# Optimization experiments

Measured on AMD Instinct MI355X. Metric: run time of the kernel, lower is better.

Reference implementation:

```python
import jax, jax.numpy as jnp
import numpy as np

K = 32        # num_classes
NQ = 16384    # num query samples
C = 512       # feature_dim
H_REF = 512   # refinement_net hidden
H_CONF = 256  # confidence_net hidden
NUM_STEPS = 3


def setup_inputs() -> dict:
    key = jax.random.key(0)
    ks = jax.random.split(key, 8)
    s = 0.02
    return {
        "prototypes": jax.random.normal(ks[0], (K, C), jnp.float32),
        "query_features": jax.random.normal(ks[1], (NQ, C), jnp.float32),
        "query_distances": jax.random.uniform(ks[2], (NQ, K), jnp.float32) * 10.0,
        "W1": jax.random.normal(ks[3], (2 * C, H_REF), jnp.float32) * s,
        "b1": jnp.zeros((H_REF,), jnp.float32),
        "W2": jax.random.normal(ks[4], (H_REF, C), jnp.float32) * s,
        "b2": jnp.zeros((C,), jnp.float32),
        "Wc1": jax.random.normal(ks[5], (2 * C, H_CONF), jnp.float32) * s,
        "bc1": jnp.zeros((H_CONF,), jnp.float32),
        "Wc2": jax.random.normal(ks[6], (H_CONF, 1), jnp.float32) * s,
        "bc2": jnp.zeros((1,), jnp.float32),
    }


def reference(prototypes, query_features, query_distances,
              W1, b1, W2, b2, Wc1, bc1, Wc2, bc2):
    # ---- refinement loop (3 steps, sequential in refined prototypes) ----
    refined = prototypes
    for step in range(NUM_STEPS):
        # soft assignments over classes; temperature = step + 1
        soft = jax.nn.softmax(-query_distances / (step + 1.0), axis=-1)  # (NQ, K)
        wsum = jnp.maximum(soft.sum(axis=0), 1e-6)                       # (K,)  clamp(min=1e-6)
        wmean = (soft.T @ query_features) / wsum[:, None]                # (K, C)
        concat = jnp.concatenate([refined, wmean], axis=-1)              # (K, 2C)
        h = jax.nn.relu(concat @ W1 + b1)                                # dropout is identity in eval
        refinement = h @ W2 + b2                                         # (K, C)
        refined = refined + 0.1 * refinement

    # ---- confidence scores: MLP on [proto, query] pairs, mean over queries ----
    # Split first-layer weight into proto half and query half to avoid
    # materializing the (K, NQ, 2C) concat explicitly (same math).
    Wp, Wq = Wc1[:C], Wc1[C:]
    hp = prototypes @ Wp          # (K, H_CONF)
    hq = query_features @ Wq      # (NQ, H_CONF)
    hidden = jax.nn.relu(hp[:, None, :] + hq[None, :, :] + bc1)  # (K, NQ, H_CONF)
    conf = jax.nn.sigmoid(hidden @ Wc2 + bc2)                    # (K, NQ, 1)
    confidence_scores = conf.reshape(K, -1).mean(axis=1)         # (K,)

    return refined, confidence_scores
```

## Files before the change

### kernel.cpp

```cpp
#include <hip/hip_runtime.h>

typedef __attribute__((ext_vector_type(8))) short short8;
typedef __attribute__((ext_vector_type(4))) short short4_t;
typedef __attribute__((ext_vector_type(8))) __bf16 bf16x8;
typedef __attribute__((ext_vector_type(4))) float floatx4;

union S8B8 { short8 s; bf16x8 b; };

__device__ __forceinline__ short f2bf(float f) {
    union { float f; unsigned u; } v; v.f = f;
    unsigned r = v.u + 0x7fffu + ((v.u >> 16) & 1u);
    return (short)(r >> 16);
}
__device__ __forceinline__ float bf2f(short s) {
    union { unsigned u; float f; } v; v.u = ((unsigned)(unsigned short)s) << 16;
    return v.f;
}
__device__ __forceinline__ float bflo(unsigned u) { return __uint_as_float(u << 16); }
__device__ __forceinline__ float bfhi(unsigned u) { return __uint_as_float(u & 0xffff0000u); }

__global__ __launch_bounds__(256) void k_A(const float* __restrict__ W1, const float* __restrict__ W2,
                                           const float* __restrict__ Wc1, const float* __restrict__ proto,
                                           const float* __restrict__ bc1,
                                           short* __restrict__ W1p, short* __restrict__ W2p,
                                           short* __restrict__ wqp, float* __restrict__ refined,
                                           float* __restrict__ wmean, float* __restrict__ hpb,
                                           int* __restrict__ bar, float* __restrict__ wsum,
                                           float* __restrict__ dout) {
    int tid = threadIdx.x, bid = blockIdx.x;
    if (bid < 32) {
        int r = bid;
        const float* pr = proto + r * 512;
        const float* wc = Wc1 + tid;
        float a0 = 0.f, a1 = 0.f, a2 = 0.f, a3 = 0.f;
#pragma unroll 4
        for (int i = 0; i < 512; i += 4) {
            float4 p4 = *(const float4*)&pr[i];
            float w0 = wc[(size_t)i * 256];
            float w1 = wc[(size_t)(i + 1) * 256];
            float w2 = wc[(size_t)(i + 2) * 256];
            float w3 = wc[(size_t)(i + 3) * 256];
            a0 += p4.x * w0;
            a1 += p4.y * w1;
            a2 += p4.z * w2;
            a3 += p4.w * w3;
        }
        hpb[r * 256 + tid] = bc1[tid] + ((a0 + a1) + (a2 + a3));
        return;
    }
    if (bid < 480) {
        int idx = (bid - 32) * 256 + tid;
        if (idx < 65536) {
            int kg = idx >> 9, n = idx & 511;
            short8 o;
#pragma unroll
            for (int j = 0; j < 8; j++) o[j] = f2bf(W1[(size_t)(kg * 8 + j) * 512 + n]);
            *(short8*)&W1p[((size_t)kg * 512 + n) * 8] = o;
        } else if (idx < 98304) {
            int j2 = idx - 65536;
            int kg = j2 >> 9, n = j2 & 511;
            short8 o;
#pragma unroll
            for (int j = 0; j < 8; j++) o[j] = f2bf(W2[(size_t)(kg * 8 + j) * 512 + n]);
            *(short8*)&W2p[((size_t)kg * 512 + n) * 8] = o;
        } else {
            int j3 = idx - 98304;
            int kg = j3 >> 8, n = j3 & 255;
            short8 o;
#pragma unroll
            for (int j = 0; j < 8; j++) o[j] = f2bf(Wc1[(size_t)(512 + kg * 8 + j) * 256 + n]);
            *(short8*)&wqp[((size_t)kg * 256 + n) * 8] = o;
        }
        return;
    }
    if (bid < 544) {
        int idx = (bid - 480) * 256 + tid;
        refined[idx] = proto[idx];
        return;
    }
    if (bid < 736) {
        int idx = (bid - 544) * 256 + tid;
        wmean[idx] = 0.f;
        return;
    }
    {
        if (tid < 96) wsum[tid] = 0.f;
        else if (tid < 104) bar[tid - 96] = 0;
        else if (tid >= 128 && tid < 160) dout[16384 + tid - 128] = 0.f;
    }
}

__global__ __launch_bounds__(256) void k_B(const float* __restrict__ qd, const float* __restrict__ qf,
                                           float* __restrict__ wmean, float* __restrict__ wsum) {
    __shared__ short soft_lds[96 * 264];
    __shared__ short B_lds[128 * 40];
    int tid = threadIdx.x;
    int kc = blockIdx.x >> 2, ns = blockIdx.x & 3;
    int qb0 = kc * 256, c0 = ns * 128;

    {
        float d[32];
        const float4* p = (const float4*)(qd + (size_t)(qb0 + tid) * 32);
#pragma unroll
        for (int j = 0; j < 8; j++) {
            float4 v = p[j];
            d[4 * j] = v.x; d[4 * j + 1] = v.y; d[4 * j + 2] = v.z; d[4 * j + 3] = v.w;
        }
#pragma unroll
        for (int s = 0; s < 3; s++) {
            float inv = -1.0f / (float)(s + 1);
            float e[32];
            float sum = 0.f;
#pragma unroll
            for (int k = 0; k < 32; k++) { e[k] = __expf(d[k] * inv); sum += e[k]; }
            float r = 1.0f / sum;
#pragma unroll
            for (int k = 0; k < 32; k++)
                soft_lds[(s * 32 + k) * 264 + tid] = f2bf(e[k] * r);
        }
    }
    __syncthreads();

    if (ns == 0 && tid < 96) {
        const short* row = &soft_lds[tid * 264];
        float ssum = 0.f;
#pragma unroll 4
        for (int j = 0; j < 32; j++) {
            short8 v = *(const short8*)&row[j * 8];
#pragma unroll
            for (int i = 0; i < 8; i++) ssum += bf2f(v[i]);
        }
        atomicAdd(&wsum[tid], ssum);
    }

    int lane = tid & 63, w = tid >> 6;
    int ml = lane & 15, q8 = lane >> 4;
    int c_l = 2 * lane, q_l = 8 * w;

    floatx4 acc[6][2];
#pragma unroll
    for (int mt = 0; mt < 6; mt++)
#pragma unroll
        for (int nt = 0; nt < 2; nt++) acc[mt][nt] = (floatx4){0.f, 0.f, 0.f, 0.f};

    for (int step = 0; step < 8; step++) {
        int qb = step * 32;
        short8 sA, sB;
#pragma unroll
        for (int i = 0; i < 8; i++) {
            float2 u = *(const float2*)&qf[(size_t)(qb0 + qb + q_l + i) * 512 + c0 + c_l];
            sA[i] = f2bf(u.x);
            sB[i] = f2bf(u.y);
        }
        __syncthreads();
        *(short8*)&B_lds[c_l * 40 + q_l] = sA;
        *(short8*)&B_lds[(c_l + 1) * 40 + q_l] = sB;
        S8B8 a[6];
#pragma unroll
        for (int mt = 0; mt < 6; mt++)
            a[mt].s = *(const short8*)&soft_lds[(mt * 16 + ml) * 264 + qb + q8 * 8];
        __syncthreads();
#pragma unroll
        for (int nt = 0; nt < 2; nt++) {
            S8B8 b; b.s = *(short8*)&B_lds[(w * 32 + nt * 16 + ml) * 40 + q8 * 8];
#pragma unroll
            for (int mt = 0; mt < 6; mt++)
                acc[mt][nt] = __builtin_amdgcn_mfma_f32_16x16x32_bf16(a[mt].b, b.b, acc[mt][nt], 0, 0, 0);
        }
    }
#pragma unroll
    for (int mt = 0; mt < 6; mt++) {
#pragma unroll
        for (int nt = 0; nt < 2; nt++) {
            int c = c0 + w * 32 + nt * 16 + ml;
#pragma unroll
            for (int r = 0; r < 4; r++) {
                int m = mt * 16 + q8 * 4 + r;
                atomicAdd(&wmean[(size_t)m * 512 + c], acc[mt][nt][r]);
            }
        }
    }
}

__device__ __forceinline__ void gbar(int* bar, int phase, int nblk) {
    __syncthreads();
    if (threadIdx.x == 0) {
        __threadfence();
        __hip_atomic_fetch_add(&bar[phase], 1, __ATOMIC_ACQ_REL, __HIP_MEMORY_SCOPE_AGENT);
        while (__hip_atomic_load(&bar[phase], __ATOMIC_ACQUIRE, __HIP_MEMORY_SCOPE_AGENT) < nblk)
            __builtin_amdgcn_s_sleep(1);
    }
    __syncthreads();
}

__global__ __launch_bounds__(256) void k_D(const float* __restrict__ wmean,
                                           const float* __restrict__ wsum,
                                           const short* __restrict__ W1p,
                                           const float* __restrict__ b1,
                                           const short* __restrict__ W2p,
                                           const float* __restrict__ b2,
                                           float* __restrict__ refined,
                                           short* __restrict__ hb,
                                           int* __restrict__ bar,
                                           const float* __restrict__ qf,
                                           const short* __restrict__ wqp,
                                           const float* __restrict__ hpb,
                                           const float* __restrict__ Wc2,
                                           const float* __restrict__ bc2p,
                                           float* __restrict__ dout) {
    __shared__ float smem[6688];
    int tid = threadIdx.x, lane = tid & 63, w = tid >> 6;
    int ml = lane & 15, q8 = lane >> 4;

    if (blockIdx.x < 16) {
        float (*red)[32][36] = (float(*)[32][36])smem;
        int nb = blockIdx.x;
        int phase = 0;
        for (int s = 0; s < 3; s++) {
            {
                const float* srcA = (w < 2) ? refined : (wmean + (size_t)s * 32 * 512 - 512);
                float iv0 = 1.f, iv1 = 1.f;
                if (w >= 2) {
                    iv0 = 1.f / fmaxf(wsum[s * 32 + ml], 1e-6f);
                    iv1 = 1.f / fmaxf(wsum[s * 32 + 16 + ml], 1e-6f);
                }
                int kw = w * 256;
                floatx4 acc[2][2];
#pragma unroll
                for (int mt = 0; mt < 2; mt++)
#pragma unroll
                    for (int nt = 0; nt < 2; nt++) acc[mt][nt] = (floatx4){0.f, 0.f, 0.f, 0.f};
                for (int st = 0; st < 8; st++) {
                    int k0 = kw + st * 32 + q8 * 8;
                    S8B8 a[2];
#pragma unroll
                    for (int mt = 0; mt < 2; mt++) {
                        float sc = mt ? iv1 : iv0;
                        const float* p = &srcA[(size_t)(mt * 16 + ml) * 512 + k0];
                        float4 f0 = *(const float4*)p;
                        float4 f1 = *(const float4*)(p + 4);
                        short8 t;
                        t[0] = f2bf(f0.x * sc); t[1] = f2bf(f0.y * sc);
                        t[2] = f2bf(f0.z * sc); t[3] = f2bf(f0.w * sc);
                        t[4] = f2bf(f1.x * sc); t[5] = f2bf(f1.y * sc);
                        t[6] = f2bf(f1.z * sc); t[7] = f2bf(f1.w * sc);
                        a[mt].s = t;
                    }
#pragma unroll
                    for (int nt = 0; nt < 2; nt++) {
                        int n = nb * 32 + nt * 16 + ml;
                        S8B8 b; b.s = *(const short8*)&W1p[((size_t)(k0 >> 3) * 512 + n) * 8];
#pragma unroll
                        for (int mt = 0; mt < 2; mt++)
                            acc[mt][nt] = __builtin_amdgcn_mfma_f32_16x16x32_bf16(a[mt].b, b.b, acc[mt][nt], 0, 0, 0);
                    }
                }
                __syncthreads();
#pragma unroll
                for (int mt = 0; mt < 2; mt++)
#pragma unroll
                    for (int nt = 0; nt < 2; nt++)
#pragma unroll
                        for (int r = 0; r < 4; r++)
                            red[w][mt * 16 + q8 * 4 + r][nt * 16 + ml] = acc[mt][nt][r];
                __syncthreads();
                int m = tid >> 3, n0 = (tid & 7) * 4;
                short4_t o;
#pragma unroll
                for (int i = 0; i < 4; i++) {
                    float v = b1[nb * 32 + n0 + i];
#pragma unroll
                    for (int w4 = 0; w4 < 4; w4++) v += red[w4][m][n0 + i];
                    o[i] = f2bf(fmaxf(v, 0.f));
                }
                *(short4_t*)&hb[(size_t)m * 512 + nb * 32 + n0] = o;
            }
            gbar(bar, phase++, 16);
            {
                int kw = w * 128;
                floatx4 acc[2][2];
#pragma unroll
                for (int mt = 0; mt < 2; mt++)
#pragma unroll
                    for (int nt = 0; nt < 2; nt++) acc[mt][nt] = (floatx4){0.f, 0.f, 0.f, 0.f};
                for (int st = 0; st < 4; st++) {
                    int k0 = kw + st * 32 + q8 * 8;
                    S8B8 a[2];
#pragma unroll
                    for (int mt = 0; mt < 2; mt++)
                        a[mt].s = *(const short8*)&hb[(size_t)(mt * 16 + ml) * 512 + k0];
#pragma unroll
                    for (int nt = 0; nt < 2; nt++) {
                        int n = nb * 32 + nt * 16 + ml;
                        S8B8 b; b.s = *(const short8*)&W2p[((size_t)(k0 >> 3) * 512 + n) * 8];
#pragma unroll
                        for (int mt = 0; mt < 2; mt++)
                            acc[mt][nt] = __builtin_amdgcn_mfma_f32_16x16x32_bf16(a[mt].b, b.b, acc[mt][nt], 0, 0, 0);
                    }
                }
                __syncthreads();
#pragma unroll
                for (int mt = 0; mt < 2; mt++)
#pragma unroll
                    for (int nt = 0; nt < 2; nt++)
#pragma unroll
                        for (int r = 0; r < 4; r++)
                            red[w][mt * 16 + q8 * 4 + r][nt * 16 + ml] = acc[mt][nt][r];
                __syncthreads();
                int m = tid >> 3, n0 = (tid & 7) * 4;
#pragma unroll
                for (int i = 0; i < 4; i++) {
                    int c = nb * 32 + n0 + i;
                    float v = b2[c];
#pragma unroll
                    for (int w4 = 0; w4 < 4; w4++) v += red[w4][m][n0 + i];
                    float val = refined[(size_t)m * 512 + c] + 0.1f * v;
                    refined[(size_t)m * 512 + c] = val;
                    if (s == 2) dout[(size_t)m * 512 + c] = val;
                }
            }
            if (s < 2) gbar(bar, phase++, 16);
        }
    } else {
        short* hq_lds = (short*)smem;
        short* hp_s   = (short*)smem + 4480;
        float* wc2s   = smem + 6400;
        float* confl  = smem + 6656;
        int q0 = (blockIdx.x - 16) * 16;

        wc2s[tid] = Wc2[tid];
        if (tid < 32) confl[tid] = 0.f;
#pragma unroll
        for (int i = 0; i < 8; i++) {
            int idx = i * 256 + tid;
            int r = idx >> 6, c = (idx & 63) * 4;
            float4 v = *(const float4*)&hpb[r * 256 + c];
            short4_t o;
            o[0] = f2bf(v.x); o[1] = f2bf(v.y); o[2] = f2bf(v.z); o[3] = f2bf(v.w);
            *(short4_t*)&hp_s[r * 260 + c] = o;
        }
        {
            floatx4 acc[4];
#pragma unroll
            for (int nt = 0; nt < 4; nt++) acc[nt] = (floatx4){0.f, 0.f, 0.f, 0.f};
            const float* qfa = qf + (size_t)(q0 + ml) * 512 + q8 * 8;
#pragma unroll 4
            for (int kc = 0; kc < 512; kc += 32) {
                float4 fa = *(const float4*)&qfa[kc];
                float4 fb = *(const float4*)&qfa[kc + 4];
                short8 t;
                t[0] = f2bf(fa.x); t[1] = f2bf(fa.y); t[2] = f2bf(fa.z); t[3] = f2bf(fa.w);
                t[4] = f2bf(fb.x); t[5] = f2bf(fb.y); t[6] = f2bf(fb.z); t[7] = f2bf(fb.w);
                S8B8 a; a.s = t;
#pragma unroll
                for (int nt = 0; nt < 4; nt++) {
                    int col = w * 64 + nt * 16 + ml;
                    S8B8 b; b.s = *(const short8*)&wqp[((size_t)((kc >> 3) + q8) * 256 + col) * 8];
                    acc[nt] = __builtin_amdgcn_mfma_f32_16x16x32_bf16(a.b, b.b, acc[nt], 0, 0, 0);
                }
            }
#pragma unroll
            for (int nt = 0; nt < 4; nt++)
#pragma unroll
                for (int r = 0; r < 4; r++)
                    hq_lds[(q8 * 4 + r) * 280 + w * 64 + nt * 16 + ml] = f2bf(acc[nt][r]);
        }
        __syncthreads();

        int q = tid & 15, kg = tid >> 4;
        int k0 = kg, k1 = kg + 16;
        float s0 = 0.f, s1 = 0.f;
        for (int h = 0; h < 256; h += 4) {
            uint2 hv = *(uint2*)&hq_lds[q * 280 + h];
            float f0 = bflo(hv.x), f1 = bfhi(hv.x), f2 = bflo(hv.y), f3 = bfhi(hv.y);
            uint2 u0 = *(uint2*)&hp_s[k0 * 260 + h];
            uint2 u1 = *(uint2*)&hp_s[k1 * 260 + h];
            float4 wv = *(float4*)&wc2s[h];
            s0 += fmaxf(bflo(u0.x) + f0, 0.f) * wv.x;
            s0 += fmaxf(bfhi(u0.x) + f1, 0.f) * wv.y;
            s0 += fmaxf(bflo(u0.y) + f2, 0.f) * wv.z;
            s0 += fmaxf(bfhi(u0.y) + f3, 0.f) * wv.w;
            s1 += fmaxf(bflo(u1.x) + f0, 0.f) * wv.x;
            s1 += fmaxf(bfhi(u1.x) + f1, 0.f) * wv.y;
            s1 += fmaxf(bflo(u1.y) + f2, 0.f) * wv.z;
            s1 += fmaxf(bfhi(u1.y) + f3, 0.f) * wv.w;
        }
        float bc2 = bc2p[0];
        float v0 = 1.f / (1.f + __expf(-(s0 + bc2)));
        float v1 = 1.f / (1.f + __expf(-(s1 + bc2)));
        atomicAdd(&confl[k0], v0);
        atomicAdd(&confl[k1], v1);
        __syncthreads();
        if (tid < 32) atomicAdd(&dout[16384 + tid], confl[tid] * (1.0f / 16384.0f));
    }
}

extern "C" void kernel_launch(void* const* d_in, const int* in_sizes, int n_in,
                              void* d_out, int out_size, void* d_ws, size_t ws_size,
                              hipStream_t stream) {
    const float* proto = (const float*)d_in[0];
    const float* qf    = (const float*)d_in[1];
    const float* qd    = (const float*)d_in[2];
    const float* W1    = (const float*)d_in[3];
    const float* b1    = (const float*)d_in[4];
    const float* W2    = (const float*)d_in[5];
    const float* b2    = (const float*)d_in[6];
    const float* Wc1   = (const float*)d_in[7];
    const float* bc1   = (const float*)d_in[8];
    const float* Wc2   = (const float*)d_in[9];
    const float* bc2   = (const float*)d_in[10];
    float* out = (float*)d_out;

    float* ws = (float*)d_ws;
    float* wmean   = ws;
    float* refined = ws + 49152;
    short* hb      = (short*)(ws + 65536);
    short* W1p     = (short*)(ws + 73728);
    short* W2p     = (short*)(ws + 335872);
    short* wqp     = (short*)(ws + 466944);
    float* hpb     = ws + 532480;
    int*   bar     = (int*)(ws + 540672);
    float* wsum    = ws + 540680;

    k_A<<<737, 256, 0, stream>>>(W1, W2, Wc1, proto, bc1, W1p, W2p, wqp,
                                 refined, wmean, hpb, bar, wsum, out);
    k_B<<<256, 256, 0, stream>>>(qd, qf, wmean, wsum);
    k_D<<<1040, 256, 0, stream>>>(wmean, wsum, W1p, b1, W2p, b2, refined, hb, bar,
                                  qf, wqp, hpb, Wc2, bc2, out);
}
```

Before: 180.3 us.

## Merge soft-assignment GEMM and refinement into one kernel with flag-based dependency

Folds the soft-assignment weighted-mean kernel into the main kernel, so the confidence-MLP blocks run concurrently with the wmean accumulation instead of after it. The refinement blocks, placed last, spin on a completion counter until all 256 wmean blocks have signalled. The wmean GEMM also drops its LDS staging of query features and loads the B fragments straight from global memory, removing two barriers per step. This cuts one kernel launch boundary and overlaps independent work. It relies on the wmean blocks being scheduled before the spinning refinement blocks to avoid deadlock, and the direct strided global loads may be less coalesced.

```diff
diff --git a/kernel.cpp b/kernel.cpp
--- a/kernel.cpp
+++ b/kernel.cpp
@@ -90,98 +90,6 @@
     }
 }
 
-__global__ __launch_bounds__(256) void k_B(const float* __restrict__ qd, const float* __restrict__ qf,
-                                           float* __restrict__ wmean, float* __restrict__ wsum) {
-    __shared__ short soft_lds[96 * 264];
-    __shared__ short B_lds[128 * 40];
-    int tid = threadIdx.x;
-    int kc = blockIdx.x >> 2, ns = blockIdx.x & 3;
-    int qb0 = kc * 256, c0 = ns * 128;
-
-    {
-        float d[32];
-        const float4* p = (const float4*)(qd + (size_t)(qb0 + tid) * 32);
-#pragma unroll
-        for (int j = 0; j < 8; j++) {
-            float4 v = p[j];
-            d[4 * j] = v.x; d[4 * j + 1] = v.y; d[4 * j + 2] = v.z; d[4 * j + 3] = v.w;
-        }
-#pragma unroll
-        for (int s = 0; s < 3; s++) {
-            float inv = -1.0f / (float)(s + 1);
-            float e[32];
-            float sum = 0.f;
-#pragma unroll
-            for (int k = 0; k < 32; k++) { e[k] = __expf(d[k] * inv); sum += e[k]; }
-            float r = 1.0f / sum;
-#pragma unroll
-            for (int k = 0; k < 32; k++)
-                soft_lds[(s * 32 + k) * 264 + tid] = f2bf(e[k] * r);
-        }
-    }
-    __syncthreads();
-
-    if (ns == 0 && tid < 96) {
-        const short* row = &soft_lds[tid * 264];
-        float ssum = 0.f;
-#pragma unroll 4
-        for (int j = 0; j < 32; j++) {
-            short8 v = *(const short8*)&row[j * 8];
-#pragma unroll
-            for (int i = 0; i < 8; i++) ssum += bf2f(v[i]);
-        }
-        atomicAdd(&wsum[tid], ssum);
-    }
-
-    int lane = tid & 63, w = tid >> 6;
-    int ml = lane & 15, q8 = lane >> 4;
-    int c_l = 2 * lane, q_l = 8 * w;
-
-    floatx4 acc[6][2];
-#pragma unroll
-    for (int mt = 0; mt < 6; mt++)
-#pragma unroll
-        for (int nt = 0; nt < 2; nt++) acc[mt][nt] = (floatx4){0.f, 0.f, 0.f, 0.f};
-
-    for (int step = 0; step < 8; step++) {
-        int qb = step * 32;
-        short8 sA, sB;
-#pragma unroll
-        for (int i = 0; i < 8; i++) {
-            float2 u = *(const float2*)&qf[(size_t)(qb0 + qb + q_l + i) * 512 + c0 + c_l];
-            sA[i] = f2bf(u.x);
-            sB[i] = f2bf(u.y);
-        }
-        __syncthreads();
-        *(short8*)&B_lds[c_l * 40 + q_l] = sA;
-        *(short8*)&B_lds[(c_l + 1) * 40 + q_l] = sB;
-        S8B8 a[6];
-#pragma unroll
-        for (int mt = 0; mt < 6; mt++)
-            a[mt].s = *(const short8*)&soft_lds[(mt * 16 + ml) * 264 + qb + q8 * 8];
-        __syncthreads();
-#pragma unroll
-        for (int nt = 0; nt < 2; nt++) {
-            S8B8 b; b.s = *(short8*)&B_lds[(w * 32 + nt * 16 + ml) * 40 + q8 * 8];
-#pragma unroll
-            for (int mt = 0; mt < 6; mt++)
-                acc[mt][nt] = __builtin_amdgcn_mfma_f32_16x16x32_bf16(a[mt].b, b.b, acc[mt][nt], 0, 0, 0);
-        }
-    }
-#pragma unroll
-    for (int mt = 0; mt < 6; mt++) {
-#pragma unroll
-        for (int nt = 0; nt < 2; nt++) {
-            int c = c0 + w * 32 + nt * 16 + ml;
-#pragma unroll
-            for (int r = 0; r < 4; r++) {
-                int m = mt * 16 + q8 * 4 + r;
-                atomicAdd(&wmean[(size_t)m * 512 + c], acc[mt][nt][r]);
-            }
-        }
-    }
-}
-
 __device__ __forceinline__ void gbar(int* bar, int phase, int nblk) {
     __syncthreads();
     if (threadIdx.x == 0) {
@@ -193,140 +101,113 @@
     __syncthreads();
 }
 
-__global__ __launch_bounds__(256) void k_D(const float* __restrict__ wmean,
-                                           const float* __restrict__ wsum,
-                                           const short* __restrict__ W1p,
-                                           const float* __restrict__ b1,
-                                           const short* __restrict__ W2p,
-                                           const float* __restrict__ b2,
-                                           float* __restrict__ refined,
-                                           short* __restrict__ hb,
+__global__ __launch_bounds__(256) void k_M(const float* __restrict__ qd, const float* __restrict__ qf,
+                                           float* __restrict__ wmean, float* __restrict__ wsum,
+                                           const short* __restrict__ W1p, const float* __restrict__ b1,
+                                           const short* __restrict__ W2p, const float* __restrict__ b2,
+                                           float* __restrict__ refined, short* __restrict__ hb,
                                            int* __restrict__ bar,
-                                           const float* __restrict__ qf,
-                                           const short* __restrict__ wqp,
-                                           const float* __restrict__ hpb,
-                                           const float* __restrict__ Wc2,
-                                           const float* __restrict__ bc2p,
+                                           const short* __restrict__ wqp, const float* __restrict__ hpb,
+                                           const float* __restrict__ Wc2, const float* __restrict__ bc2p,
                                            float* __restrict__ dout) {
-    __shared__ float smem[6688];
+    __shared__ float smem[12672];
     int tid = threadIdx.x, lane = tid & 63, w = tid >> 6;
     int ml = lane & 15, q8 = lane >> 4;
-
-    if (blockIdx.x < 16) {
-        float (*red)[32][36] = (float(*)[32][36])smem;
-        int nb = blockIdx.x;
-        int phase = 0;
-        for (int s = 0; s < 3; s++) {
-            {
-                const float* srcA = (w < 2) ? refined : (wmean + (size_t)s * 32 * 512 - 512);
-                float iv0 = 1.f, iv1 = 1.f;
-                if (w >= 2) {
-                    iv0 = 1.f / fmaxf(wsum[s * 32 + ml], 1e-6f);
-                    iv1 = 1.f / fmaxf(wsum[s * 32 + 16 + ml], 1e-6f);
-                }
-                int kw = w * 256;
-                floatx4 acc[2][2];
-#pragma unroll
-                for (int mt = 0; mt < 2; mt++)
-#pragma unroll
-                    for (int nt = 0; nt < 2; nt++) acc[mt][nt] = (floatx4){0.f, 0.f, 0.f, 0.f};
-                for (int st = 0; st < 8; st++) {
-                    int k0 = kw + st * 32 + q8 * 8;
-                    S8B8 a[2];
-#pragma unroll
-                    for (int mt = 0; mt < 2; mt++) {
-                        float sc = mt ? iv1 : iv0;
-                        const float* p = &srcA[(size_t)(mt * 16 + ml) * 512 + k0];
-                        float4 f0 = *(const float4*)p;
-                        float4 f1 = *(const float4*)(p + 4);
-                        short8 t;
-                        t[0] = f2bf(f0.x * sc); t[1] = f2bf(f0.y * sc);
-                        t[2] = f2bf(f0.z * sc); t[3] = f2bf(f0.w * sc);
-                        t[4] = f2bf(f1.x * sc); t[5] = f2bf(f1.y * sc);
-                        t[6] = f2bf(f1.z * sc); t[7] = f2bf(f1.w * sc);
-                        a[mt].s = t;
-                    }
-#pragma unroll
-                    for (int nt = 0; nt < 2; nt++) {
-                        int n = nb * 32 + nt * 16 + ml;
-                        S8B8 b; b.s = *(const short8*)&W1p[((size_t)(k0 >> 3) * 512 + n) * 8];
-#pragma unroll
-                        for (int mt = 0; mt < 2; mt++)
-                            acc[mt][nt] = __builtin_amdgcn_mfma_f32_16x16x32_bf16(a[mt].b, b.b, acc[mt][nt], 0, 0, 0);
-                    }
-                }
-                __syncthreads();
-#pragma unroll
-                for (int mt = 0; mt < 2; mt++)
-#pragma unroll
-                    for (int nt = 0; nt < 2; nt++)
-#pragma unroll
-                        for (int r = 0; r < 4; r++)
-                            red[w][mt * 16 + q8 * 4 + r][nt * 16 + ml] = acc[mt][nt][r];
-                __syncthreads();
-                int m = tid >> 3, n0 = (tid & 7) * 4;
-                short4_t o;
-#pragma unroll
-                for (int i = 0; i < 4; i++) {
-                    float v = b1[nb * 32 + n0 + i];
-#pragma unroll
-                    for (int w4 = 0; w4 < 4; w4++) v += red[w4][m][n0 + i];
-                    o[i] = f2bf(fmaxf(v, 0.f));
-                }
-                *(short4_t*)&hb[(size_t)m * 512 + nb * 32 + n0] = o;
-            }
-            gbar(bar, phase++, 16);
-            {
-                int kw = w * 128;
-                floatx4 acc[2][2];
-#pragma unroll
-                for (int mt = 0; mt < 2; mt++)
-#pragma unroll
-                    for (int nt = 0; nt < 2; nt++) acc[mt][nt] = (floatx4){0.f, 0.f, 0.f, 0.f};
-                for (int st = 0; st < 4; st++) {
-                    int k0 = kw + st * 32 + q8 * 8;
-                    S8B8 a[2];
-#pragma unroll
-                    for (int mt = 0; mt < 2; mt++)
-                        a[mt].s = *(const short8*)&hb[(size_t)(mt * 16 + ml) * 512 + k0];
-#pragma unroll
-                    for (int nt = 0; nt < 2; nt++) {
-                        int n = nb * 32 + nt * 16 + ml;
-                        S8B8 b; b.s = *(const short8*)&W2p[((size_t)(k0 >> 3) * 512 + n) * 8];
-#pragma unroll
-                        for (int mt = 0; mt < 2; mt++)
-                            acc[mt][nt] = __builtin_amdgcn_mfma_f32_16x16x32_bf16(a[mt].b, b.b, acc[mt][nt], 0, 0, 0);
-                    }
-                }
-                __syncthreads();
-#pragma unroll
-                for (int mt = 0; mt < 2; mt++)
-#pragma unroll
-                    for (int nt = 0; nt < 2; nt++)
-#pragma unroll
-                        for (int r = 0; r < 4; r++)
-                            red[w][mt * 16 + q8 * 4 + r][nt * 16 + ml] = acc[mt][nt][r];
-                __syncthreads();
-                int m = tid >> 3, n0 = (tid & 7) * 4;
-#pragma unroll
-                for (int i = 0; i < 4; i++) {
-                    int c = nb * 32 + n0 + i;
-                    float v = b2[c];
-#pragma unroll
-                    for (int w4 = 0; w4 < 4; w4++) v += red[w4][m][n0 + i];
-                    float val = refined[(size_t)m * 512 + c] + 0.1f * v;
-                    refined[(size_t)m * 512 + c] = val;
-                    if (s == 2) dout[(size_t)m * 512 + c] = val;
-                }
-            }
-            if (s < 2) gbar(bar, phase++, 16);
-        }
-    } else {
+    int bid = blockIdx.x;
+
+    if (bid < 256) {
+        short* soft_lds = (short*)smem;
+        int kc = bid >> 2, ns = bid & 3;
+        int qb0 = kc * 256, c0 = ns * 128;
+        {
+            float d[32];
+            const float4* p = (const float4*)(qd + (size_t)(qb0 + tid) * 32);
+#pragma unroll
+            for (int j = 0; j < 8; j++) {
+                float4 v = p[j];
+                d[4 * j] = v.x; d[4 * j + 1] = v.y; d[4 * j + 2] = v.z; d[4 * j + 3] = v.w;
+            }
+#pragma unroll
+            for (int s = 0; s < 3; s++) {
+                float inv = -1.0f / (float)(s + 1);
+                float e[32];
+                float sum = 0.f;
+#pragma unroll
+                for (int k = 0; k < 32; k++) { e[k] = __expf(d[k] * inv); sum += e[k]; }
+                float r = 1.0f / sum;
+#pragma unroll
+                for (int k = 0; k < 32; k++)
+                    soft_lds[(s * 32 + k) * 264 + tid] = f2bf(e[k] * r);
+            }
+        }
+        __syncthreads();
+
+        if (ns == 0 && tid < 96) {
+            const short* row = &soft_lds[tid * 264];
+            float ssum = 0.f;
+#pragma unroll 4
+            for (int j = 0; j < 32; j++) {
+                short8 v = *(const short8*)&row[j * 8];
+#pragma unroll
+                for (int i = 0; i < 8; i++) ssum += bf2f(v[i]);
+            }
+            atomicAdd(&wsum[tid], ssum);
+        }
+
+        floatx4 acc[6][2];
+#pragma unroll
+        for (int mt = 0; mt < 6; mt++)
+#pragma unroll
+            for (int nt = 0; nt < 2; nt++) acc[mt][nt] = (floatx4){0.f, 0.f, 0.f, 0.f};
+
+        for (int step = 0; step < 8; step++) {
+            int qb = step * 32;
+            S8B8 a[6];
+#pragma unroll
+            for (int mt = 0; mt < 6; mt++)
+                a[mt].s = *(const short8*)&soft_lds[(mt * 16 + ml) * 264 + qb + q8 * 8];
+            S8B8 bfr[2];
+#pragma unroll
+            for (int nt = 0; nt < 2; nt++) {
+                int c = c0 + w * 32 + nt * 16 + ml;
+                const float* qp = &qf[(size_t)(qb0 + qb + q8 * 8) * 512 + c];
+                short8 t;
+#pragma unroll
+                for (int i = 0; i < 8; i++) t[i] = f2bf(qp[(size_t)i * 512]);
+                bfr[nt].s = t;
+            }
+#pragma unroll
+            for (int nt = 0; nt < 2; nt++)
+#pragma unroll
+                for (int mt = 0; mt < 6; mt++)
+                    acc[mt][nt] = __builtin_amdgcn_mfma_f32_16x16x32_bf16(a[mt].b, bfr[nt].b, acc[mt][nt], 0, 0, 0);
+        }
+#pragma unroll
+        for (int mt = 0; mt < 6; mt++) {
+#pragma unroll
+            for (int nt = 0; nt < 2; nt++) {
+                int c = c0 + w * 32 + nt * 16 + ml;
+#pragma unroll
+                for (int r = 0; r < 4; r++) {
+                    int m = mt * 16 + q8 * 4 + r;
+                    atomicAdd(&wmean[(size_t)m * 512 + c], acc[mt][nt][r]);
+                }
+            }
+        }
+        __syncthreads();
+        if (tid == 0) {
+            __threadfence();
+            __hip_atomic_fetch_add(&bar[6], 1, __ATOMIC_ACQ_REL, __HIP_MEMORY_SCOPE_AGENT);
+        }
+        return;
+    }
+
+    if (bid < 1280) {
         short* hq_lds = (short*)smem;
         short* hp_s   = (short*)smem + 4480;
         float* wc2s   = smem + 6400;
         float* confl  = smem + 6656;
-        int q0 = (blockIdx.x - 16) * 16;
+        int q0 = (bid - 256) * 16;
 
         wc2s[tid] = Wc2[tid];
         if (tid < 32) confl[tid] = 0.f;
@@ -392,6 +273,123 @@
         atomicAdd(&confl[k1], v1);
         __syncthreads();
         if (tid < 32) atomicAdd(&dout[16384 + tid], confl[tid] * (1.0f / 16384.0f));
+        return;
+    }
+
+    if (tid == 0) {
+        while (__hip_atomic_load(&bar[6], __ATOMIC_ACQUIRE, __HIP_MEMORY_SCOPE_AGENT) < 256)
+            __builtin_amdgcn_s_sleep(1);
+    }
+    __syncthreads();
+    {
+        float (*red)[32][36] = (float(*)[32][36])smem;
+        int nb = bid - 1280;
+        int phase = 0;
+        for (int s = 0; s < 3; s++) {
+            {
+                const float* srcA = (w < 2) ? refined : (wmean + (size_t)s * 32 * 512 - 512);
+                float iv0 = 1.f, iv1 = 1.f;
+                if (w >= 2) {
+                    iv0 = 1.f / fmaxf(wsum[s * 32 + ml], 1e-6f);
+                    iv1 = 1.f / fmaxf(wsum[s * 32 + 16 + ml], 1e-6f);
+                }
+                int kw = w * 256;
+                floatx4 acc[2][2];
+#pragma unroll
+                for (int mt = 0; mt < 2; mt++)
+#pragma unroll
+                    for (int nt = 0; nt < 2; nt++) acc[mt][nt] = (floatx4){0.f, 0.f, 0.f, 0.f};
+                for (int st = 0; st < 8; st++) {
+                    int k0 = kw + st * 32 + q8 * 8;
+                    S8B8 a[2];
+#pragma unroll
+                    for (int mt = 0; mt < 2; mt++) {
+                        float sc = mt ? iv1 : iv0;
+                        const float* p = &srcA[(size_t)(mt * 16 + ml) * 512 + k0];
+                        float4 f0 = *(const float4*)p;
+                        float4 f1 = *(const float4*)(p + 4);
+                        short8 t;
+                        t[0] = f2bf(f0.x * sc); t[1] = f2bf(f0.y * sc);
+                        t[2] = f2bf(f0.z * sc); t[3] = f2bf(f0.w * sc);
+                        t[4] = f2bf(f1.x * sc); t[5] = f2bf(f1.y * sc);
+                        t[6] = f2bf(f1.z * sc); t[7] = f2bf(f1.w * sc);
+                        a[mt].s = t;
+                    }
+#pragma unroll
+                    for (int nt = 0; nt < 2; nt++) {
+                        int n = nb * 32 + nt * 16 + ml;
+                        S8B8 b; b.s = *(const short8*)&W1p[((size_t)(k0 >> 3) * 512 + n) * 8];
+#pragma unroll
+                        for (int mt = 0; mt < 2; mt++)
+                            acc[mt][nt] = __builtin_amdgcn_mfma_f32_16x16x32_bf16(a[mt].b, b.b, acc[mt][nt], 0, 0, 0);
+                    }
+                }
+                __syncthreads();
+#pragma unroll
+                for (int mt = 0; mt < 2; mt++)
+#pragma unroll
+                    for (int nt = 0; nt < 2; nt++)
+#pragma unroll
+                        for (int r = 0; r < 4; r++)
+                            red[w][mt * 16 + q8 * 4 + r][nt * 16 + ml] = acc[mt][nt][r];
+                __syncthreads();
+                int m = tid >> 3, n0 = (tid & 7) * 4;
+                short4_t o;
+#pragma unroll
+                for (int i = 0; i < 4; i++) {
+                    float v = b1[nb * 32 + n0 + i];
+#pragma unroll
+                    for (int w4 = 0; w4 < 4; w4++) v += red[w4][m][n0 + i];
+                    o[i] = f2bf(fmaxf(v, 0.f));
+                }
+                *(short4_t*)&hb[(size_t)m * 512 + nb * 32 + n0] = o;
+            }
+            gbar(bar, phase++, 16);
+            {
+                int kw = w * 128;
+                floatx4 acc[2][2];
+#pragma unroll
+                for (int mt = 0; mt < 2; mt++)
+#pragma unroll
+                    for (int nt = 0; nt < 2; nt++) acc[mt][nt] = (floatx4){0.f, 0.f, 0.f, 0.f};
+                for (int st = 0; st < 4; st++) {
+                    int k0 = kw + st * 32 + q8 * 8;
+                    S8B8 a[2];
+#pragma unroll
+                    for (int mt = 0; mt < 2; mt++)
+                        a[mt].s = *(const short8*)&hb[(size_t)(mt * 16 + ml) * 512 + k0];
+#pragma unroll
+                    for (int nt = 0; nt < 2; nt++) {
+                        int n = nb * 32 + nt * 16 + ml;
+                        S8B8 b; b.s = *(const short8*)&W2p[((size_t)(k0 >> 3) * 512 + n) * 8];
+#pragma unroll
+                        for (int mt = 0; mt < 2; mt++)
+                            acc[mt][nt] = __builtin_amdgcn_mfma_f32_16x16x32_bf16(a[mt].b, b.b, acc[mt][nt], 0, 0, 0);
+                    }
+                }
+                __syncthreads();
+#pragma unroll
+                for (int mt = 0; mt < 2; mt++)
+#pragma unroll
+                    for (int nt = 0; nt < 2; nt++)
+#pragma unroll
+                        for (int r = 0; r < 4; r++)
+                            red[w][mt * 16 + q8 * 4 + r][nt * 16 + ml] = acc[mt][nt][r];
+                __syncthreads();
+                int m = tid >> 3, n0 = (tid & 7) * 4;
+#pragma unroll
+                for (int i = 0; i < 4; i++) {
+                    int c = nb * 32 + n0 + i;
+                    float v = b2[c];
+#pragma unroll
+                    for (int w4 = 0; w4 < 4; w4++) v += red[w4][m][n0 + i];
+                    float val = refined[(size_t)m * 512 + c] + 0.1f * v;
+                    refined[(size_t)m * 512 + c] = val;
+                    if (s == 2) dout[(size_t)m * 512 + c] = val;
+                }
+            }
+            if (s < 2) gbar(bar, phase++, 16);
+        }
     }
 }
 
@@ -424,7 +422,6 @@
 
     k_A<<<737, 256, 0, stream>>>(W1, W2, Wc1, proto, bc1, W1p, W2p, wqp,
                                  refined, wmean, hpb, bar, wsum, out);
-    k_B<<<256, 256, 0, stream>>>(qd, qf, wmean, wsum);
-    k_D<<<1040, 256, 0, stream>>>(wmean, wsum, W1p, b1, W2p, b2, refined, hb, bar,
-                                  qf, wqp, hpb, Wc2, bc2, out);
-}
+    k_M<<<1296, 256, 0, stream>>>(qd, qf, wmean, wsum, W1p, b1, W2p, b2, refined, hb, bar,
+                                  wqp, hpb, Wc2, bc2, out);
+}
```

New measurement: 247.1 us. 37.1% more time.
